# Kernel tuning notes

Measured on AMD Instinct MI355X. Metric: run time of the kernel, lower is better.

The kernel has to match this reference:

```python
import jax, jax.numpy as jnp
import numpy as np

BETA = 10.0    # ste surrogate-gradient scale (module default beta=10)
SLOPE = 1.0
GAMMA = 100.0  # trigger sharpness (module default gamma=100)
EPS = 1e-30

# Straight-through estimator: hard threshold forward, sigmoid-derivative surrogate backward
@jax.custom_vjp
def ste(v):
    return (v > 0).astype(v.dtype)

def _ste_fwd(v):
    return ste(v), v

def _ste_bwd(v, g):
    e = jnp.exp(-SLOPE * v)
    return (BETA * g * SLOPE * e / ((e + 1.0) ** 2 + EPS),)

ste.defvjp(_ste_fwd, _ste_bwd)


def setup_inputs() -> dict:
    key = jax.random.key(0)
    k1, k2, k3 = jax.random.split(key, 3)
    B, I, O = 256, 1024, 1024
    ACT_RATIO = 0.1
    x = jax.random.normal(k1, (B, I), dtype=jnp.float32)
    v_weight = jax.random.uniform(k2, (O, I), dtype=jnp.float32) - (1.0 - ACT_RATIO)
    # fc weight: xavier uniform
    bound = float(np.sqrt(6.0 / (I + O)))
    fc_weight = jax.random.uniform(k3, (O, I), dtype=jnp.float32, minval=-bound, maxval=bound)
    return {"x": x, "v_weight": v_weight, "fc_weight": fc_weight}


def reference(x, v_weight, fc_weight):
    # x: [B, I]; v_weight, fc_weight: [O, I]
    mask = ste(v_weight)                        # [O, I], 0/1 child mask
    x_en = x[:, None, :] * mask                 # [B, O, I] (x_enlarge * ste(v))
    w = fc_weight * mask                        # [O, I] masked matmul weight
    y = x @ w.T                                 # [B, O]
    # trigger value: tanh(gamma*|x|) where child, 1 where not; prod over input dim
    delta_en = jnp.tanh(GAMMA * jnp.abs(x_en)) * mask + (1.0 - mask)  # [B, O, I]
    delta = jnp.prod(delta_en, axis=-1)         # [B, O]
    y = jax.nn.relu(y * delta)
    return (y, delta)
```

## Files before the change

### kernel.cpp

```cpp
#include <hip/hip_runtime.h>
#include <cmath>

#define B_ 256
#define I_ 1024
#define O_ 1024

typedef __attribute__((ext_vector_type(8))) short short8;
typedef __attribute__((ext_vector_type(4))) float f32x4;

__device__ inline unsigned short f2bf(float f) {
  union { float f; unsigned u; } c;
  c.f = f;
  unsigned u = c.u;
  return (unsigned short)((u + 0x7FFFu + ((u >> 16) & 1u)) >> 16);
}

#define WBLKS ((O_ * I_) / 2048)
#define XBLKS ((B_ * I_) / 2048)

__global__ __launch_bounds__(256) void prep_all(
    const float* __restrict__ x, const float* __restrict__ vw,
    const float* __restrict__ fcw, unsigned short* __restrict__ xb,
    unsigned short* __restrict__ ltb, unsigned short* __restrict__ wb,
    unsigned short* __restrict__ mb) {
  const int bid = blockIdx.x;
  if (bid < WBLKS) {
    int idx = (bid * 256 + threadIdx.x) * 8;
    float4 v0 = *reinterpret_cast<const float4*>(vw + idx);
    float4 v1 = *reinterpret_cast<const float4*>(vw + idx + 4);
    float4 f0 = *reinterpret_cast<const float4*>(fcw + idx);
    float4 f1 = *reinterpret_cast<const float4*>(fcw + idx + 4);
    float va[8] = {v0.x, v0.y, v0.z, v0.w, v1.x, v1.y, v1.z, v1.w};
    float fa[8] = {f0.x, f0.y, f0.z, f0.w, f1.x, f1.y, f1.z, f1.w};
    short8 wv, mv;
#pragma unroll
    for (int j = 0; j < 8; ++j) {
      bool m = va[j] > 0.0f;
      wv[j] = (short)f2bf(m ? fa[j] : 0.0f);
      mv[j] = (short)(m ? 0x3F80 : 0x0000);
    }
    *reinterpret_cast<short8*>(wb + idx) = wv;
    *reinterpret_cast<short8*>(mb + idx) = mv;
  } else {
    int idx = ((bid - WBLKS) * 256 + threadIdx.x) * 8;
    float4 x0 = *reinterpret_cast<const float4*>(x + idx);
    float4 x1 = *reinterpret_cast<const float4*>(x + idx + 4);
    float xa[8] = {x0.x, x0.y, x0.z, x0.w, x1.x, x1.y, x1.z, x1.w};
    short8 xv, lv;
#pragma unroll
    for (int j = 0; j < 8; ++j) {
      xv[j] = (short)f2bf(xa[j]);
      float l = fmaxf(logf(tanhf(100.0f * fabsf(xa[j]))), -1e30f);
      lv[j] = (short)f2bf(l);
    }
    *reinterpret_cast<short8*>(xb + idx) = xv;
    *reinterpret_cast<short8*>(ltb + idx) = lv;
  }
}

__global__ __launch_bounds__(256) void mfma_fused(
    const unsigned short* __restrict__ xb, const unsigned short* __restrict__ ltb,
    const unsigned short* __restrict__ wb, const unsigned short* __restrict__ mb,
    float* __restrict__ out) {
  const int on0 = blockIdx.x * 32;
  const int bm0 = blockIdx.y * 32;

  __shared__ short As[32][72];
  __shared__ short Ls[32][72];
  __shared__ short Ws[32][72];
  __shared__ short Ms[32][72];

  const int t = threadIdx.x;
  const int lane = t & 63;
  const int wid = t >> 6;
  const int wm = wid >> 1, wn = wid & 1;
  const int lr = lane & 15;
  const int lk = (lane >> 4) * 8;

  const int srow = t >> 3;
  const int scol = (t & 7) * 8;

  const size_t aoff = (size_t)(bm0 + srow) * I_ + scol;
  const size_t boff = (size_t)(on0 + srow) * I_ + scol;

  short8 rx = *reinterpret_cast<const short8*>(xb + aoff);
  short8 rl = *reinterpret_cast<const short8*>(ltb + aoff);
  short8 rw = *reinterpret_cast<const short8*>(wb + boff);
  short8 rm = *reinterpret_cast<const short8*>(mb + boff);

  f32x4 accd = {0.f, 0.f, 0.f, 0.f};
  f32x4 accs = {0.f, 0.f, 0.f, 0.f};

  for (int kt = 0; kt < I_; kt += 64) {
    __syncthreads();
    *reinterpret_cast<short8*>(&As[srow][scol]) = rx;
    *reinterpret_cast<short8*>(&Ls[srow][scol]) = rl;
    *reinterpret_cast<short8*>(&Ws[srow][scol]) = rw;
    *reinterpret_cast<short8*>(&Ms[srow][scol]) = rm;
    if (kt + 64 < I_) {
      rx = *reinterpret_cast<const short8*>(xb + aoff + kt + 64);
      rl = *reinterpret_cast<const short8*>(ltb + aoff + kt + 64);
      rw = *reinterpret_cast<const short8*>(wb + boff + kt + 64);
      rm = *reinterpret_cast<const short8*>(mb + boff + kt + 64);
    }
    __syncthreads();
#pragma unroll
    for (int ks = 0; ks < 2; ++ks) {
      const int kb = ks * 32 + lk;
      short8 af = *reinterpret_cast<const short8*>(&As[wm * 16 + lr][kb]);
      short8 lf = *reinterpret_cast<const short8*>(&Ls[wm * 16 + lr][kb]);
      short8 wf = *reinterpret_cast<const short8*>(&Ws[wn * 16 + lr][kb]);
      short8 mf = *reinterpret_cast<const short8*>(&Ms[wn * 16 + lr][kb]);
      accd = __builtin_amdgcn_mfma_f32_16x16x32_bf16(af, wf, accd, 0, 0, 0);
      accs = __builtin_amdgcn_mfma_f32_16x16x32_bf16(lf, mf, accs, 0, 0, 0);
    }
  }

  const int orow = bm0 + wm * 16 + (lane >> 4) * 4;
  const int ocol = on0 + wn * 16 + lr;
#pragma unroll
  for (int r = 0; r < 4; ++r) {
    float d = expf(accs[r]);
    float y = fmaxf(accd[r] * d, 0.0f);
    size_t off = (size_t)(orow + r) * O_ + ocol;
    out[off] = y;
    out[(size_t)B_ * O_ + off] = d;
  }
}

__global__ __launch_bounds__(256) void dual_gemm_f32(
    const float* __restrict__ x, const float* __restrict__ vw,
    const float* __restrict__ fcw, float* __restrict__ out) {
  const int on0 = blockIdx.x * 64;
  const int bm0 = blockIdx.y * 64;
  __shared__ float xs[32][68];
  __shared__ float ls[32][68];
  __shared__ float wsm[32][68];
  __shared__ float msh[32][68];
  const int t = threadIdx.x;
  const int tx = t & 15, ty = t >> 4;
  const int m0 = ty * 4, n0 = tx * 4;
  float accd[4][4] = {{0.f}};
  float accs[4][4] = {{0.f}};
  for (int kt = 0; kt < I_; kt += 32) {
#pragma unroll
    for (int j = 0; j < 8; ++j) {
      int f = j * 256 + t;
      int m = f >> 5;
      int kk = f & 31;
      int gk = kt + kk;
      float xv = x[(size_t)(bm0 + m) * I_ + gk];
      xs[kk][m] = xv;
      ls[kk][m] = fmaxf(logf(tanhf(100.0f * fabsf(xv))), -1e30f);
      float vv = vw[(size_t)(on0 + m) * I_ + gk];
      float fv = fcw[(size_t)(on0 + m) * I_ + gk];
      float mk = vv > 0.0f ? 1.0f : 0.0f;
      wsm[kk][m] = fv * mk;
      msh[kk][m] = mk;
    }
    __syncthreads();
#pragma unroll
    for (int kk = 0; kk < 32; ++kk) {
      float4 xv = *reinterpret_cast<const float4*>(&xs[kk][m0]);
      float4 lv = *reinterpret_cast<const float4*>(&ls[kk][m0]);
      float4 wv = *reinterpret_cast<const float4*>(&wsm[kk][n0]);
      float4 mv = *reinterpret_cast<const float4*>(&msh[kk][n0]);
      float xa[4] = {xv.x, xv.y, xv.z, xv.w};
      float la[4] = {lv.x, lv.y, lv.z, lv.w};
      float wa[4] = {wv.x, wv.y, wv.z, wv.w};
      float ma[4] = {mv.x, mv.y, mv.z, mv.w};
#pragma unroll
      for (int i = 0; i < 4; ++i)
#pragma unroll
        for (int j = 0; j < 4; ++j) {
          accd[i][j] = fmaf(xa[i], wa[j], accd[i][j]);
          accs[i][j] = fmaf(la[i], ma[j], accs[i][j]);
        }
    }
    __syncthreads();
  }
#pragma unroll
  for (int i = 0; i < 4; ++i) {
    int row = bm0 + m0 + i;
#pragma unroll
    for (int j = 0; j < 4; ++j) {
      float delta = expf(accs[i][j]);
      out[(size_t)row * O_ + on0 + n0 + j] = fmaxf(accd[i][j] * delta, 0.0f);
      out[(size_t)B_ * O_ + (size_t)row * O_ + on0 + n0 + j] = delta;
    }
  }
}

extern "C" void kernel_launch(void* const* d_in, const int* in_sizes, int n_in,
                              void* d_out, int out_size, void* d_ws,
                              size_t ws_size, hipStream_t stream) {
  const float* x = (const float*)d_in[0];
  const float* vw = (const float*)d_in[1];
  const float* fcw = (const float*)d_in[2];
  float* out = (float*)d_out;

  const size_t xbB = (size_t)B_ * I_ * 2;
  const size_t wbB = (size_t)O_ * I_ * 2;
  const size_t bfB = 2 * xbB + 2 * wbB;

  unsigned short* xb = (unsigned short*)d_ws;
  unsigned short* ltb = (unsigned short*)((char*)d_ws + xbB);
  unsigned short* wb = (unsigned short*)((char*)d_ws + 2 * xbB);
  unsigned short* mb = (unsigned short*)((char*)d_ws + 2 * xbB + wbB);

  if (ws_size >= bfB) {
    prep_all<<<WBLKS + XBLKS, 256, 0, stream>>>(x, vw, fcw, xb, ltb, wb, mb);
    mfma_fused<<<dim3(O_ / 32, B_ / 32), 256, 0, stream>>>(xb, ltb, wb, mb, out);
  } else {
    dual_gemm_f32<<<dim3(O_ / 64, B_ / 64, 1), 256, 0, stream>>>(x, vw, fcw, out);
  }
}
```

Measured before the change: 17.93 us.

## Split K across two wave groups per block with LDS reduction

The fused MFMA kernel now launches 512 threads per block, and each 256-thread half handles one half of the reduction dimension in its own shared-memory buffer. The halves then combine their partial dot-product and log-sum accumulators through shared memory before the exp/relu epilogue. The aim is to halve the serial K-loop length per block and raise wave parallelism on a grid that has only 256 blocks. In exchange it doubles shared memory per block and adds a reduction step with extra barriers.

```diff
diff --git a/kernel.cpp b/kernel.cpp
--- a/kernel.cpp
+++ b/kernel.cpp
@@ -58,30 +58,32 @@
   }
 }
 
-__global__ __launch_bounds__(256) void mfma_fused(
+__global__ __launch_bounds__(512) void mfma_fused2(
     const unsigned short* __restrict__ xb, const unsigned short* __restrict__ ltb,
     const unsigned short* __restrict__ wb, const unsigned short* __restrict__ mb,
     float* __restrict__ out) {
   const int on0 = blockIdx.x * 32;
   const int bm0 = blockIdx.y * 32;
 
-  __shared__ short As[32][72];
-  __shared__ short Ls[32][72];
-  __shared__ short Ws[32][72];
-  __shared__ short Ms[32][72];
+  __shared__ short As[2][32][72];
+  __shared__ short Ls[2][32][72];
+  __shared__ short Ws[2][32][72];
+  __shared__ short Ms[2][32][72];
 
   const int t = threadIdx.x;
   const int lane = t & 63;
   const int wid = t >> 6;
-  const int wm = wid >> 1, wn = wid & 1;
+  const int kg = wid >> 2;
+  const int wm = (wid >> 1) & 1, wn = wid & 1;
   const int lr = lane & 15;
   const int lk = (lane >> 4) * 8;
 
-  const int srow = t >> 3;
-  const int scol = (t & 7) * 8;
-
-  const size_t aoff = (size_t)(bm0 + srow) * I_ + scol;
-  const size_t boff = (size_t)(on0 + srow) * I_ + scol;
+  const int tl = t & 255;
+  const int srow = tl >> 3;
+  const int scol = (tl & 7) * 8;
+
+  const size_t aoff = (size_t)(bm0 + srow) * I_ + kg * 512 + scol;
+  const size_t boff = (size_t)(on0 + srow) * I_ + kg * 512 + scol;
 
   short8 rx = *reinterpret_cast<const short8*>(xb + aoff);
   short8 rl = *reinterpret_cast<const short8*>(ltb + aoff);
@@ -91,13 +93,13 @@
   f32x4 accd = {0.f, 0.f, 0.f, 0.f};
   f32x4 accs = {0.f, 0.f, 0.f, 0.f};
 
-  for (int kt = 0; kt < I_; kt += 64) {
-    __syncthreads();
-    *reinterpret_cast<short8*>(&As[srow][scol]) = rx;
-    *reinterpret_cast<short8*>(&Ls[srow][scol]) = rl;
-    *reinterpret_cast<short8*>(&Ws[srow][scol]) = rw;
-    *reinterpret_cast<short8*>(&Ms[srow][scol]) = rm;
-    if (kt + 64 < I_) {
+  for (int kt = 0; kt < 512; kt += 64) {
+    __syncthreads();
+    *reinterpret_cast<short8*>(&As[kg][srow][scol]) = rx;
+    *reinterpret_cast<short8*>(&Ls[kg][srow][scol]) = rl;
+    *reinterpret_cast<short8*>(&Ws[kg][srow][scol]) = rw;
+    *reinterpret_cast<short8*>(&Ms[kg][srow][scol]) = rm;
+    if (kt + 64 < 512) {
       rx = *reinterpret_cast<const short8*>(xb + aoff + kt + 64);
       rl = *reinterpret_cast<const short8*>(ltb + aoff + kt + 64);
       rw = *reinterpret_cast<const short8*>(wb + boff + kt + 64);
@@ -107,24 +109,39 @@
 #pragma unroll
     for (int ks = 0; ks < 2; ++ks) {
       const int kb = ks * 32 + lk;
-      short8 af = *reinterpret_cast<const short8*>(&As[wm * 16 + lr][kb]);
-      short8 lf = *reinterpret_cast<const short8*>(&Ls[wm * 16 + lr][kb]);
-      short8 wf = *reinterpret_cast<const short8*>(&Ws[wn * 16 + lr][kb]);
-      short8 mf = *reinterpret_cast<const short8*>(&Ms[wn * 16 + lr][kb]);
+      short8 af = *reinterpret_cast<const short8*>(&As[kg][wm * 16 + lr][kb]);
+      short8 lf = *reinterpret_cast<const short8*>(&Ls[kg][wm * 16 + lr][kb]);
+      short8 wf = *reinterpret_cast<const short8*>(&Ws[kg][wn * 16 + lr][kb]);
+      short8 mf = *reinterpret_cast<const short8*>(&Ms[kg][wn * 16 + lr][kb]);
       accd = __builtin_amdgcn_mfma_f32_16x16x32_bf16(af, wf, accd, 0, 0, 0);
       accs = __builtin_amdgcn_mfma_f32_16x16x32_bf16(lf, mf, accs, 0, 0, 0);
     }
   }
 
-  const int orow = bm0 + wm * 16 + (lane >> 4) * 4;
-  const int ocol = on0 + wn * 16 + lr;
-#pragma unroll
-  for (int r = 0; r < 4; ++r) {
-    float d = expf(accs[r]);
-    float y = fmaxf(accd[r] * d, 0.0f);
-    size_t off = (size_t)(orow + r) * O_ + ocol;
-    out[off] = y;
-    out[(size_t)B_ * O_ + off] = d;
+  __syncthreads();
+  float* red = reinterpret_cast<float*>(&As[0][0][0]);
+  const int ridx = ((wid & 3) * 64 + lane) * 8;
+  if (kg == 1) {
+#pragma unroll
+    for (int r = 0; r < 4; ++r) {
+      red[ridx + r] = accd[r];
+      red[ridx + 4 + r] = accs[r];
+    }
+  }
+  __syncthreads();
+  if (kg == 0) {
+    const int orow = bm0 + wm * 16 + (lane >> 4) * 4;
+    const int ocol = on0 + wn * 16 + lr;
+#pragma unroll
+    for (int r = 0; r < 4; ++r) {
+      float dsum = accd[r] + red[ridx + r];
+      float ssum = accs[r] + red[ridx + 4 + r];
+      float d = expf(ssum);
+      float y = fmaxf(dsum * d, 0.0f);
+      size_t off = (size_t)(orow + r) * O_ + ocol;
+      out[off] = y;
+      out[(size_t)B_ * O_ + off] = d;
+    }
   }
 }
 
@@ -210,7 +227,7 @@
 
   if (ws_size >= bfB) {
     prep_all<<<WBLKS + XBLKS, 256, 0, stream>>>(x, vw, fcw, xb, ltb, wb, mb);
-    mfma_fused<<<dim3(O_ / 32, B_ / 32), 256, 0, stream>>>(xb, ltb, wb, mb, out);
+    mfma_fused2<<<dim3(O_ / 32, B_ / 32), 512, 0, stream>>>(xb, ltb, wb, mb, out);
   } else {
     dual_gemm_f32<<<dim3(O_ / 64, B_ / 64, 1), 256, 0, stream>>>(x, vw, fcw, out);
   }
```

New measurement: 16.78 us. 1.07x faster.
